# Kernel tuning notes

Hardware: AMD Instinct MI355X
Metric: run time of the kernel (lower is better)

## Reference

```python
import jax, jax.numpy as jnp
import numpy as np

STATE_MASS = 4.0
EPS = 1e-5
LOW_RANK_SCALE = 0.1  # _LOW_RANK_SCALE_INIT


def _ln(x, g, b):
    mu = jnp.mean(x, axis=-1, keepdims=True)
    var = jnp.var(x, axis=-1, keepdims=True)
    return (x - mu) * jax.lax.rsqrt(var + EPS) * g + b


def _signed_abs_softmax(s, axis=-1):
    s = jnp.nan_to_num(s)
    return jnp.sign(s) * jax.nn.softmax(jnp.abs(s), axis=axis)


def _signed_softmax_state(st):
    st = jnp.nan_to_num(st)
    return jnp.sign(st) * jax.nn.softmax(jnp.abs(st), axis=-1) * STATE_MASS


def _low_rank_scores(dst, src, Ut_w, Ut_b, Us_w, Us_b, w):
    # bilinear low-rank pairwise: score[b,i,j] = sum_r (dst_i Ut)_r * w_r * (src_j Us)_r
    pt = dst @ Ut_w + Ut_b                      # [B,Nd,R]
    ps = src @ Us_w + Us_b                      # [B,Ns,R]
    return jnp.einsum('bir,r,bjr->bij', pt, w * LOW_RANK_SCALE, ps)


def _gather_rows(x, idx):
    # x: [B,N,...], idx: [B,M,K] -> [B,M,K,...] (per-batch gather, no NxM broadcast)
    return jax.vmap(lambda xi, ii: xi[ii])(x, idx)


def setup_inputs() -> dict:
    key = jax.random.key(0)
    ks = jax.random.split(key, 8)
    B, S, D, M, R = 16, 2048, 512, 256, 64
    std = 0.02
    return {
        'token_val': jax.random.normal(ks[0], (B, S, D), jnp.float32),
        'token_state': jax.random.normal(ks[1], (B, S), jnp.float32),
        'init_state': jax.random.normal(ks[2], (M,), jnp.float32) * std,
        'init_val': jax.random.normal(ks[3], (M, D), jnp.float32) * std,
        'rUs_w': jax.random.normal(ks[4], (D, R), jnp.float32) * std,
        'rUs_b': jnp.zeros((R,), jnp.float32),
        'rUt_w': jax.random.normal(ks[5], (D, R), jnp.float32) * std,
        'rUt_b': jnp.zeros((R,), jnp.float32),
        'r_w': jnp.ones((R,), jnp.float32),
        'pUs_w': jax.random.normal(ks[6], (D, R), jnp.float32) * std,
        'pUs_b': jnp.zeros((R,), jnp.float32),
        'pUt_w': jax.random.normal(ks[7], (D, R), jnp.float32) * std,
        'pUt_b': jnp.zeros((R,), jnp.float32),
        'p_w': jnp.ones((R,), jnp.float32),
        'ln_g': jnp.ones((D,), jnp.float32),
        'ln_b': jnp.zeros((D,), jnp.float32),
        'topk': 16,
    }


def reference(token_val, token_state, init_state, init_val,
              rUs_w, rUs_b, rUt_w, rUt_b, r_w,
              pUs_w, pUs_b, pUt_w, pUt_b, p_w,
              ln_g, ln_b, topk):
    B = token_val.shape[0]
    M, D = init_val.shape

    # _MemoryLevel.initialize
    mem_state = _signed_softmax_state(jnp.broadcast_to(init_state, (B, M)))
    mem_val = _ln(jnp.broadcast_to(init_val, (B, M, D)), ln_g, ln_b)

    # ---- SparseTransition (write): route tokens -> slots, top-k sources/slot ----
    scores = _low_rank_scores(mem_val, token_val, rUt_w, rUt_b, rUs_w, rUs_b, r_w)  # [B,M,S]
    _, idx = jax.lax.top_k(jnp.abs(scores), topk)              # [B,M,K]
    sel = jnp.take_along_axis(scores, idx, axis=-1)            # [B,M,K]
    edges = _signed_abs_softmax(sel, axis=-1)                  # signed-abs-softmax over edges
    v_sel = _gather_rows(token_val, idx)                       # [B,M,K,D]
    s_sel = _gather_rows(token_state, idx)                     # [B,M,K]
    mem_val = mem_val + jnp.einsum('bmk,bmkd->bmd', edges, v_sel)   # merge_mode='add'
    mem_state = mem_state + jnp.einsum('bmk,bmk->bm', edges, s_sel)
    mem_state = _signed_softmax_state(mem_state)
    mem_val = _ln(mem_val, ln_g, ln_b)

    # ---- SparsePropagation within slots: state-weighted top-k edges, residual ----
    pscores = _low_rank_scores(mem_val, mem_val, pUt_w, pUt_b, pUs_w, pUs_b, p_w)   # [B,M,M]
    pscores = pscores * mem_state[:, None, :]                  # state_weight_edges
    _, pidx = jax.lax.top_k(jnp.abs(pscores), topk)            # [B,M,K]
    psel = jnp.take_along_axis(pscores, pidx, axis=-1)
    pe = _signed_abs_softmax(psel, axis=-1)
    pv = _gather_rows(mem_val, pidx)                           # [B,M,K,D]
    pst = _gather_rows(mem_state, pidx)                        # [B,M,K]
    mem_val = mem_val + jnp.einsum('bmk,bmkd->bmd', pe, pv)    # residual=True
    mem_state = mem_state + jnp.einsum('bmk,bmk->bm', pe, pst)
    mem_state = _signed_softmax_state(mem_state)
    mem_val = _ln(mem_val, ln_g, ln_b)
    return mem_val
```

## Files before the change

kernel.cpp:

```cpp
#include <hip/hip_runtime.h>
#include <hip/hip_bf16.h>
#include <math.h>

#define BB 16
#define SS 2048
#define DD 512
#define MM 256
#define RR 64
#define KK 16
#define GPAD 68

__device__ __forceinline__ float wave_sum(float v) {
#pragma unroll
  for (int off = 32; off > 0; off >>= 1) v += __shfl_xor(v, off);
  return v;
}

__device__ __forceinline__ float sgnf(float v) {
  return (v > 0.f) ? 1.f : ((v < 0.f) ? -1.f : 0.f);
}

__global__ __launch_bounds__(256) void k_init(
    const float* __restrict__ init_val, const float* __restrict__ ln_g,
    const float* __restrict__ ln_b, const float* __restrict__ rUt_w,
    const float* __restrict__ rUt_b, const float* __restrict__ r_w,
    float* __restrict__ mv0, float* __restrict__ pt0) {
  int m = blockIdx.x, t = threadIdx.x;
  __shared__ float row[DD];
  __shared__ float red[8];
  float x0 = init_val[m * DD + t];
  float x1 = init_val[m * DD + t + 256];
  float s = wave_sum(x0 + x1);
  float sq = wave_sum(x0 * x0 + x1 * x1);
  if ((t & 63) == 0) { red[t >> 6] = s; red[4 + (t >> 6)] = sq; }
  __syncthreads();
  float mean = (red[0] + red[1] + red[2] + red[3]) * (1.0f / DD);
  float var = (red[4] + red[5] + red[6] + red[7]) * (1.0f / DD) - mean * mean;
  float rs = rsqrtf(var + 1e-5f);
  float n0 = (x0 - mean) * rs * ln_g[t] + ln_b[t];
  float n1 = (x1 - mean) * rs * ln_g[t + 256] + ln_b[t + 256];
  mv0[m * DD + t] = n0;
  mv0[m * DD + t + 256] = n1;
  row[t] = n0;
  row[t + 256] = n1;
  __syncthreads();
  if (t < RR) {
    float acc = rUt_b[t];
    for (int d = 0; d < DD; ++d) acc += row[d] * rUt_w[d * RR + t];
    pt0[m * RR + t] = acc * r_w[t] * 0.1f;
  }
}

__global__ __launch_bounds__(256) void k_state_softmax(
    const float* __restrict__ in, float* __restrict__ out) {
  int b = blockIdx.x, t = threadIdx.x;
  __shared__ float red[4];
  float v = in[b * MM + t];
  float a = fabsf(v);
  float mx = a;
#pragma unroll
  for (int off = 32; off > 0; off >>= 1) mx = fmaxf(mx, __shfl_xor(mx, off));
  if ((t & 63) == 0) red[t >> 6] = mx;
  __syncthreads();
  mx = fmaxf(fmaxf(red[0], red[1]), fmaxf(red[2], red[3]));
  __syncthreads();
  float e = expf(a - mx);
  float ssum = wave_sum(e);
  if ((t & 63) == 0) red[t >> 6] = ssum;
  __syncthreads();
  ssum = red[0] + red[1] + red[2] + red[3];
  out[b * MM + t] = sgnf(v) * e / ssum * 4.0f;
}

__global__ __launch_bounds__(64) void k_ps(
    const float* __restrict__ A, const float* __restrict__ W,
    const float* __restrict__ bias, float* __restrict__ C0,
    float* __restrict__ C1, float* __restrict__ C2, float* __restrict__ C3) {
  __shared__ float Ast[8][32];
  int t = threadIdx.x;
  int rg = t >> 3;
  int cg = t & 7;
  int q = blockIdx.x >> 10;
  int rt = blockIdx.x & 1023;
  int row0 = rt * 32;
  int k0 = q * 128;
  float* C = (q == 0) ? C0 : (q == 1) ? C1 : (q == 2) ? C2 : C3;
  int lr = t >> 1;
  int ks = (t & 1) * 4;
  float acc[4][8] = {};
  for (int ch = 0; ch < 16; ++ch) {
    int kc = k0 + ch * 8;
    float4 av4 = *reinterpret_cast<const float4*>(
        &A[(size_t)(row0 + lr) * DD + kc + ks]);
    float4 wlo[8], whi[8];
#pragma unroll
    for (int j = 0; j < 8; ++j) {
      const float* wr = W + (size_t)(kc + j) * RR + cg * 8;
      wlo[j] = *reinterpret_cast<const float4*>(wr);
      whi[j] = *reinterpret_cast<const float4*>(wr + 4);
    }
    __syncthreads();
    Ast[ks + 0][lr] = av4.x;
    Ast[ks + 1][lr] = av4.y;
    Ast[ks + 2][lr] = av4.z;
    Ast[ks + 3][lr] = av4.w;
    __syncthreads();
#pragma unroll
    for (int j = 0; j < 8; ++j) {
      float4 a4 = *reinterpret_cast<const float4*>(&Ast[j][rg * 4]);
      float wv[8] = {wlo[j].x, wlo[j].y, wlo[j].z, wlo[j].w,
                     whi[j].x, whi[j].y, whi[j].z, whi[j].w};
      float av[4] = {a4.x, a4.y, a4.z, a4.w};
#pragma unroll
      for (int i = 0; i < 4; ++i)
#pragma unroll
        for (int c = 0; c < 8; ++c) acc[i][c] += av[i] * wv[c];
    }
  }
  float bvx[8];
#pragma unroll
  for (int c = 0; c < 8; ++c) bvx[c] = (q == 0) ? bias[cg * 8 + c] : 0.f;
#pragma unroll
  for (int i = 0; i < 4; ++i) {
    int rr = row0 + rg * 4 + i;
    float4 o0, o1;
    o0.x = acc[i][0] + bvx[0]; o0.y = acc[i][1] + bvx[1];
    o0.z = acc[i][2] + bvx[2]; o0.w = acc[i][3] + bvx[3];
    o1.x = acc[i][4] + bvx[4]; o1.y = acc[i][5] + bvx[5];
    o1.z = acc[i][6] + bvx[6]; o1.w = acc[i][7] + bvx[7];
    *reinterpret_cast<float4*>(&C[(size_t)rr * RR + cg * 8]) = o0;
    *reinterpret_cast<float4*>(&C[(size_t)rr * RR + cg * 8 + 4]) = o1;
  }
}

template <bool TRANS_OUT>
__device__ __forceinline__ void gemm_body(
    const float* __restrict__ A, const float* __restrict__ W,
    const float* __restrict__ bias, const float* __restrict__ colscale,
    float csmul, const float* __restrict__ rowscale, float* __restrict__ C,
    int row0, float (*Ast)[GPAD], float (*Ws)[GPAD]) {
  int tid = threadIdx.x;
  int ty = tid >> 4, tx = tid & 15;
  float acc[4][4] = {};
  for (int kc = 0; kc < DD; kc += 32) {
#pragma unroll
    for (int i = 0; i < 2; ++i) {
      int s4 = i * 256 + tid;
      int r = s4 >> 3;
      int k4 = s4 & 7;
      float4 v = *reinterpret_cast<const float4*>(
          &A[(size_t)(row0 + r) * DD + kc + k4 * 4]);
      Ast[k4 * 4 + 0][r] = v.x;
      Ast[k4 * 4 + 1][r] = v.y;
      Ast[k4 * 4 + 2][r] = v.z;
      Ast[k4 * 4 + 3][r] = v.w;
    }
#pragma unroll
    for (int i = 0; i < 2; ++i) {
      int s4 = i * 256 + tid;
      int r = s4 >> 4;
      int c4 = s4 & 15;
      float4 v = *reinterpret_cast<const float4*>(
          &W[(size_t)(kc + r) * RR + c4 * 4]);
      *reinterpret_cast<float4*>(&Ws[r][c4 * 4]) = v;
    }
    __syncthreads();
#pragma unroll
    for (int k = 0; k < 32; ++k) {
      float4 a4 = *reinterpret_cast<const float4*>(&Ast[k][ty * 4]);
      float4 w4 = *reinterpret_cast<const float4*>(&Ws[k][tx * 4]);
      acc[0][0] += a4.x * w4.x; acc[0][1] += a4.x * w4.y;
      acc[0][2] += a4.x * w4.z; acc[0][3] += a4.x * w4.w;
      acc[1][0] += a4.y * w4.x; acc[1][1] += a4.y * w4.y;
      acc[1][2] += a4.y * w4.z; acc[1][3] += a4.y * w4.w;
      acc[2][0] += a4.z * w4.x; acc[2][1] += a4.z * w4.y;
      acc[2][2] += a4.z * w4.z; acc[2][3] += a4.z * w4.w;
      acc[3][0] += a4.w * w4.x; acc[3][1] += a4.w * w4.y;
      acc[3][2] += a4.w * w4.z; acc[3][3] += a4.w * w4.w;
    }
    __syncthreads();
  }
#pragma unroll
  for (int i = 0; i < 4; ++i) {
    int rr = row0 + ty * 4 + i;
    float rsc = rowscale ? rowscale[rr] : 1.f;
#pragma unroll
    for (int j = 0; j < 4; ++j) {
      int cc = tx * 4 + j;
      float v = acc[i][j] + bias[cc];
      if (colscale) v *= colscale[cc] * csmul;
      v *= rsc;
      if (TRANS_OUT) {
        C[((size_t)(rr >> 8) * RR + cc) * MM + (rr & 255)] = v;
      } else {
        C[(size_t)rr * RR + cc] = v;
      }
    }
  }
}

__global__ __launch_bounds__(256) void k_gemm_pair(
    const float* __restrict__ mv1, const float* __restrict__ pUt_w,
    const float* __restrict__ pUt_b, const float* __restrict__ p_w,
    const float* __restrict__ pUs_w, const float* __restrict__ pUs_b,
    const float* __restrict__ ms1, float* __restrict__ pt1,
    float* __restrict__ ps1T) {
  __shared__ float Ast[32][GPAD];
  __shared__ float Ws[32][GPAD];
  if (blockIdx.x < 64) {
    gemm_body<false>(mv1, pUt_w, pUt_b, p_w, 0.1f, nullptr, pt1,
                     blockIdx.x * 64, Ast, Ws);
  } else {
    gemm_body<true>(mv1, pUs_w, pUs_b, nullptr, 1.f, ms1, ps1T,
                    (blockIdx.x - 64) * 64, Ast, Ws);
  }
}

#define PSW 144
__device__ __forceinline__ int psw(int j) { return j + ((j >> 5) << 2); }

__global__ __launch_bounds__(256) void k_scores(
    const float* __restrict__ pt0, const float* __restrict__ ps0,
    const float* __restrict__ ps1, const float* __restrict__ ps2,
    const float* __restrict__ ps3, float* __restrict__ scores) {
  __shared__ float PtT[RR][128];
  __shared__ float PsT[RR][PSW];
  int t = threadIdx.x;
  int b = blockIdx.z;
  int m0 = blockIdx.y * 128;
  int j0 = blockIdx.x * 128;
#pragma unroll
  for (int ii = 0; ii < 2; ++ii) {
    int slot = ii * 256 + t;
    int tm4 = slot >> 4, tk4 = slot & 15;
    const float* base = pt0 + (size_t)(m0 + tm4 * 4) * RR + tk4 * 4;
    float4 v0 = *reinterpret_cast<const float4*>(base);
    float4 v1 = *reinterpret_cast<const float4*>(base + RR);
    float4 v2 = *reinterpret_cast<const float4*>(base + 2 * RR);
    float4 v3 = *reinterpret_cast<const float4*>(base + 3 * RR);
    float4 w;
    w.x = v0.x; w.y = v1.x; w.z = v2.x; w.w = v3.x;
    *reinterpret_cast<float4*>(&PtT[tk4 * 4 + 0][tm4 * 4]) = w;
    w.x = v0.y; w.y = v1.y; w.z = v2.y; w.w = v3.y;
    *reinterpret_cast<float4*>(&PtT[tk4 * 4 + 1][tm4 * 4]) = w;
    w.x = v0.z; w.y = v1.z; w.z = v2.z; w.w = v3.z;
    *reinterpret_cast<float4*>(&PtT[tk4 * 4 + 2][tm4 * 4]) = w;
    w.x = v0.w; w.y = v1.w; w.z = v2.w; w.w = v3.w;
    *reinterpret_cast<float4*>(&PtT[tk4 * 4 + 3][tm4 * 4]) = w;
  }
#pragma unroll
  for (int ii = 0; ii < 2; ++ii) {
    int slot = ii * 256 + t;
    int jt = slot >> 4, kt = slot & 15;
    size_t off = ((size_t)b * SS + j0 + jt * 4) * RR + kt * 4;
    float4 v0, v1, v2, v3;
    {
      const float* p0 = ps0 + off;
      const float* p1 = ps1 + off;
      const float* p2 = ps2 + off;
      const float* p3 = ps3 + off;
#pragma unroll
      for (int rr2 = 0; rr2 < 4; ++rr2) {
        float4 a = *reinterpret_cast<const float4*>(p0 + rr2 * RR);
        float4 bq = *reinterpret_cast<const float4*>(p1 + rr2 * RR);
        float4 cq = *reinterpret_cast<const float4*>(p2 + rr2 * RR);
        float4 dq = *reinterpret_cast<const float4*>(p3 + rr2 * RR);
        float4 r;
        r.x = a.x + bq.x + cq.x + dq.x;
        r.y = a.y + bq.y + cq.y + dq.y;
        r.z = a.z + bq.z + cq.z + dq.z;
        r.w = a.w + bq.w + cq.w + dq.w;
        if (rr2 == 0) v0 = r; else if (rr2 == 1) v1 = r;
        else if (rr2 == 2) v2 = r; else v3 = r;
      }
    }
    int jc = psw(jt * 4);
    float4 w;
    w.x = v0.x; w.y = v1.x; w.z = v2.x; w.w = v3.x;
    *reinterpret_cast<float4*>(&PsT[kt * 4 + 0][jc]) = w;
    w.x = v0.y; w.y = v1.y; w.z = v2.y; w.w = v3.y;
    *reinterpret_cast<float4*>(&PsT[kt * 4 + 1][jc]) = w;
    w.x = v0.z; w.y = v1.z; w.z = v2.z; w.w = v3.z;
    *reinterpret_cast<float4*>(&PsT[kt * 4 + 2][jc]) = w;
    w.x = v0.w; w.y = v1.w; w.z = v2.w; w.w = v3.w;
    *reinterpret_cast<float4*>(&PsT[kt * 4 + 3][jc]) = w;
  }
  __syncthreads();
  int jg = t & 15;
  int mg = t >> 4;
  int jlo = psw(jg * 8);
  float acc[8][8] = {};
#pragma unroll
  for (int k = 0; k < RR; ++k) {
    float4 a0 = *reinterpret_cast<const float4*>(&PtT[k][mg * 8]);
    float4 a1 = *reinterpret_cast<const float4*>(&PtT[k][mg * 8 + 4]);
    float4 w0 = *reinterpret_cast<const float4*>(&PsT[k][jlo]);
    float4 w1 = *reinterpret_cast<const float4*>(&PsT[k][jlo + 4]);
    float av[8] = {a0.x, a0.y, a0.z, a0.w, a1.x, a1.y, a1.z, a1.w};
    float wv[8] = {w0.x, w0.y, w0.z, w0.w, w1.x, w1.y, w1.z, w1.w};
#pragma unroll
    for (int r = 0; r < 8; ++r)
#pragma unroll
      for (int cc = 0; cc < 8; ++cc) acc[r][cc] += av[r] * wv[cc];
  }
  float* obase =
      scores + (size_t)b * MM * SS + (size_t)(m0 + mg * 8) * SS + j0 + jg * 8;
#pragma unroll
  for (int r = 0; r < 8; ++r) {
    float4 o0, o1;
    o0.x = acc[r][0]; o0.y = acc[r][1]; o0.z = acc[r][2]; o0.w = acc[r][3];
    o1.x = acc[r][4]; o1.y = acc[r][5]; o1.z = acc[r][6]; o1.w = acc[r][7];
    *reinterpret_cast<float4*>(obase + (size_t)r * SS) = o0;
    *reinterpret_cast<float4*>(obase + (size_t)r * SS + 4) = o1;
  }
}

__global__ __launch_bounds__(256) void k_write(
    const float* __restrict__ scores, const float* __restrict__ token_val,
    const float* __restrict__ token_state, const float* __restrict__ mv0,
    const float* __restrict__ ms0, const float* __restrict__ ln_g,
    const float* __restrict__ ln_b, float* __restrict__ mv1,
    float* __restrict__ ms_w) {
  int t = threadIdx.x;
  int wave = t >> 6, lane = t & 63;
  int i = blockIdx.x;
  int slot = i >> 3;
  int b = 2 * (i & 7) + (slot >> 6);
  int m = (slot & 63) * 4 + wave;
  int row = b * MM + m;
  __shared__ float srl[4][SS];
  __shared__ int selj_sh[4][KK];
  float4* srl4 = reinterpret_cast<float4*>(&srl[wave][0]);
  const float* srow = scores + (size_t)row * SS;
  unsigned au[32];
  unsigned maxa = 0u;
#pragma unroll
  for (int ch = 0; ch < 8; ++ch) {
    float4 q = *reinterpret_cast<const float4*>(srow + (ch * 64 + lane) * 4);
    srl4[ch * 64 + lane] = q;
    au[ch * 4 + 0] = __float_as_uint(q.x) & 0x7fffffffu;
    au[ch * 4 + 1] = __float_as_uint(q.y) & 0x7fffffffu;
    au[ch * 4 + 2] = __float_as_uint(q.z) & 0x7fffffffu;
    au[ch * 4 + 3] = __float_as_uint(q.w) & 0x7fffffffu;
    maxa = max(maxa, max(max(au[ch * 4], au[ch * 4 + 1]),
                         max(au[ch * 4 + 2], au[ch * 4 + 3])));
  }
#pragma unroll
  for (int off = 32; off > 0; off >>= 1)
    maxa = max(maxa, (unsigned)__shfl_xor((int)maxa, off));
  unsigned lo = 0u, hi = maxa, thr = 0u;
  bool early = false;
  while (lo < hi) {
    unsigned mid = lo + ((hi - lo + 1u) >> 1);
    int cnt = 0;
#pragma unroll
    for (int c = 0; c < 32; ++c) cnt += __popcll(__ballot(au[c] >= mid));
    if (cnt == KK) { thr = mid; early = true; break; }
    if (cnt > KK) lo = mid; else hi = mid - 1u;
  }
  if (!early) thr = lo;
  unsigned long long ltmask = (1ull << lane) - 1ull;
  int s = 0;
  unsigned tiemask = 0u;
#pragma unroll
  for (int c = 0; c < 32; ++c) {
    bool sg = early ? (au[c] >= thr) : (au[c] > thr);
    unsigned long long mk = __ballot(sg);
    if (sg)
      selj_sh[wave][s + __popcll(mk & ltmask)] =
          (c >> 2) * 256 + lane * 4 + (c & 3);
    s += __popcll(mk);
    if (!early && au[c] == thr) tiemask |= 1u << c;
  }
  int taken = s;
  while (taken < KK) {
    int myj = 0x7fffffff;
#pragma unroll
    for (int c = 0; c < 32; ++c)
      if ((tiemask >> c) & 1u) {
        int j = (c >> 2) * 256 + lane * 4 + (c & 3);
        myj = min(myj, j);
      }
    int wj = myj;
#pragma unroll
    for (int off = 32; off > 0; off >>= 1) wj = min(wj, __shfl_xor(wj, off));
    if (wj == 0x7fffffff) break;
    if (((wj >> 2) & 63) == lane) tiemask &= ~(1u << (((wj >> 8) << 2) | (wj & 3)));
    if (lane == 0) selj_sh[wave][taken] = wj;
    ++taken;
  }
  int js[KK];
  float es[KK];
#pragma unroll
  for (int k = 0; k < KK; ++k) {
    js[k] = selj_sh[wave][k];
    es[k] = srl[wave][js[k]];
  }
  float mx = 0.f;
#pragma unroll
  for (int k = 0; k < KK; ++k) mx = fmaxf(mx, fabsf(es[k]));
  float ssum = 0.f;
#pragma unroll
  for (int k = 0; k < KK; ++k) {
    float ex = expf(fabsf(es[k]) - mx);
    ssum += ex;
    es[k] = sgnf(es[k]) * ex;
  }
  float inv = 1.f / ssum;
  int dbase = lane * 8;
  const float* m0row = mv0 + m * DD + dbase;
  float4 a0 = *reinterpret_cast<const float4*>(m0row);
  float4 a1 = *reinterpret_cast<const float4*>(m0row + 4);
  float acc[8] = {a0.x, a0.y, a0.z, a0.w, a1.x, a1.y, a1.z, a1.w};
  float stacc = 0.f;
#pragma unroll
  for (int k = 0; k < KK; ++k) {
    float e = es[k] * inv;
    const float* tv = token_val + ((size_t)b * SS + js[k]) * DD + dbase;
    float4 u0 = *reinterpret_cast<const float4*>(tv);
    float4 u1 = *reinterpret_cast<const float4*>(tv + 4);
    acc[0] += e * u0.x; acc[1] += e * u0.y; acc[2] += e * u0.z; acc[3] += e * u0.w;
    acc[4] += e * u1.x; acc[5] += e * u1.y; acc[6] += e * u1.z; acc[7] += e * u1.w;
    stacc += e * token_state[(size_t)b * SS + js[k]];
  }
  if (lane == 0) ms_w[row] = ms0[m] + stacc;
  float s1 = 0.f, s2 = 0.f;
#pragma unroll
  for (int c = 0; c < 8; ++c) { s1 += acc[c]; s2 += acc[c] * acc[c]; }
  s1 = wave_sum(s1);
  s2 = wave_sum(s2);
  float mean = s1 * (1.0f / DD);
  float var = s2 * (1.0f / DD) - mean * mean;
  float rs = rsqrtf(var + 1e-5f);
  float4 g0 = *reinterpret_cast<const float4*>(ln_g + dbase);
  float4 g1 = *reinterpret_cast<const float4*>(ln_g + dbase + 4);
  float4 b0v = *reinterpret_cast<const float4*>(ln_b + dbase);
  float4 b1v = *reinterpret_cast<const float4*>(ln_b + dbase + 4);
  float4 o0, o1;
  o0.x = (acc[0] - mean) * rs * g0.x + b0v.x;
  o0.y = (acc[1] - mean) * rs * g0.y + b0v.y;
  o0.z = (acc[2] - mean) * rs * g0.z + b0v.z;
  o0.w = (acc[3] - mean) * rs * g0.w + b0v.w;
  o1.x = (acc[4] - mean) * rs * g1.x + b1v.x;
  o1.y = (acc[5] - mean) * rs * g1.y + b1v.y;
  o1.z = (acc[6] - mean) * rs * g1.z + b1v.z;
  o1.w = (acc[7] - mean) * rs * g1.w + b1v.w;
  float* orow = mv1 + (size_t)row * DD + dbase;
  *reinterpret_cast<float4*>(orow) = o0;
  *reinterpret_cast<float4*>(orow + 4) = o1;
}

__global__ __launch_bounds__(256, 4) void k_prop(
    const float* __restrict__ pt1, const float* __restrict__ ps1T,
    const float* __restrict__ mv1, const float* __restrict__ ln_g,
    const float* __restrict__ ln_b, float* __restrict__ out) {
  int t = threadIdx.x;
  int wave = t >> 6, lane = t & 63;
  int row = blockIdx.x * 4 + wave;
  int b = row >> 8, m = row & 255;
  __shared__ int selj_sh[4][KK];
  __shared__ float selv_sh[4][KK];
  float ptval = pt1[(size_t)row * RR + lane];
  const float* pB = ps1T + (size_t)b * RR * MM + lane * 4;
  float sc[4] = {0.f, 0.f, 0.f, 0.f};
#pragma unroll 8
  for (int r = 0; r < RR; ++r) {
    float w = __shfl(ptval, r);
    float4 pv = *reinterpret_cast<const float4*>(pB + r * MM);
    sc[0] += w * pv.x; sc[1] += w * pv.y; sc[2] += w * pv.z; sc[3] += w * pv.w;
  }
  int jbase = lane * 4;
  unsigned au[4];
#pragma unroll
  for (int c = 0; c < 4; ++c) au[c] = __float_as_uint(sc[c]) & 0x7fffffffu;
  unsigned lo = 0u, hi = 0x7f800000u, thr = 0u;
  bool early = false;
  while (lo < hi) {
    unsigned mid = lo + ((hi - lo + 1u) >> 1);
    int cnt = 0;
#pragma unroll
    for (int c = 0; c < 4; ++c) cnt += __popcll(__ballot(au[c] >= mid));
    if (cnt == KK) { thr = mid; early = true; break; }
    if (cnt > KK) lo = mid; else hi = mid - 1u;
  }
  if (!early) thr = lo;
  unsigned long long ltmask = (1ull << lane) - 1ull;
  int s = 0;
  unsigned tiemask = 0u;
#pragma unroll
  for (int c = 0; c < 4; ++c) {
    bool sg = early ? (au[c] >= thr) : (au[c] > thr);
    unsigned long long mk = __ballot(sg);
    if (sg) {
      int slot = s + __popcll(mk & ltmask);
      selj_sh[wave][slot] = jbase + c;
      selv_sh[wave][slot] = sc[c];
    }
    s += __popcll(mk);
    if (!early && au[c] == thr) tiemask |= 1u << c;
  }
  int taken = s;
  while (taken < KK) {
    int myj = 0x7fffffff;
#pragma unroll
    for (int c = 0; c < 4; ++c)
      if ((tiemask >> c) & 1u) myj = min(myj, jbase + c);
    int wj = myj;
#pragma unroll
    for (int off = 32; off > 0; off >>= 1) wj = min(wj, __shfl_xor(wj, off));
    if (wj == 0x7fffffff) break;
    if (wj >= jbase && wj < jbase + 4) {
      tiemask &= ~(1u << (wj - jbase));
      selv_sh[wave][taken] = sc[wj - jbase];
      if (lane == (wj >> 2)) selj_sh[wave][taken] = wj;
    }
    ++taken;
  }
  int js[KK];
  float es[KK];
#pragma unroll
  for (int k = 0; k < KK; ++k) { js[k] = selj_sh[wave][k]; es[k] = selv_sh[wave][k]; }
  float mx = 0.f;
#pragma unroll
  for (int k = 0; k < KK; ++k) mx = fmaxf(mx, fabsf(es[k]));
  float ssum = 0.f;
#pragma unroll
  for (int k = 0; k < KK; ++k) {
    float ex = expf(fabsf(es[k]) - mx);
    ssum += ex;
    es[k] = sgnf(es[k]) * ex;
  }
  float inv = 1.f / ssum;
  int dbase = lane * 8;
  const float* mrow = mv1 + (size_t)row * DD + dbase;
  float4 a0 = *reinterpret_cast<const float4*>(mrow);
  float4 a1 = *reinterpret_cast<const float4*>(mrow + 4);
  float acc[8] = {a0.x, a0.y, a0.z, a0.w, a1.x, a1.y, a1.z, a1.w};
#pragma unroll
  for (int k = 0; k < KK; ++k) {
    float e = es[k] * inv;
    const float* pv = mv1 + ((size_t)b * MM + js[k]) * DD + dbase;
    float4 u0 = *reinterpret_cast<const float4*>(pv);
    float4 u1 = *reinterpret_cast<const float4*>(pv + 4);
    acc[0] += e * u0.x; acc[1] += e * u0.y; acc[2] += e * u0.z; acc[3] += e * u0.w;
    acc[4] += e * u1.x; acc[5] += e * u1.y; acc[6] += e * u1.z; acc[7] += e * u1.w;
  }
  float s1 = 0.f, s2 = 0.f;
#pragma unroll
  for (int c = 0; c < 8; ++c) { s1 += acc[c]; s2 += acc[c] * acc[c]; }
  s1 = wave_sum(s1);
  s2 = wave_sum(s2);
  float mean = s1 * (1.0f / DD);
  float var = s2 * (1.0f / DD) - mean * mean;
  float rs = rsqrtf(var + 1e-5f);
  float4 g0 = *reinterpret_cast<const float4*>(ln_g + dbase);
  float4 g1 = *reinterpret_cast<const float4*>(ln_g + dbase + 4);
  float4 b0v = *reinterpret_cast<const float4*>(ln_b + dbase);
  float4 b1v = *reinterpret_cast<const float4*>(ln_b + dbase + 4);
  float4 o0, o1;
  o0.x = (acc[0] - mean) * rs * g0.x + b0v.x;
  o0.y = (acc[1] - mean) * rs * g0.y + b0v.y;
  o0.z = (acc[2] - mean) * rs * g0.z + b0v.z;
  o0.w = (acc[3] - mean) * rs * g0.w + b0v.w;
  o1.x = (acc[4] - mean) * rs * g1.x + b1v.x;
  o1.y = (acc[5] - mean) * rs * g1.y + b1v.y;
  o1.z = (acc[6] - mean) * rs * g1.z + b1v.z;
  o1.w = (acc[7] - mean) * rs * g1.w + b1v.w;
  float* orow = out + (size_t)row * DD + dbase;
  *reinterpret_cast<float4*>(orow) = o0;
  *reinterpret_cast<float4*>(orow + 4) = o1;
}

extern "C" void kernel_launch(void* const* d_in, const int* in_sizes, int n_in,
                              void* d_out, int out_size, void* d_ws,
                              size_t ws_size, hipStream_t stream) {
  const float* token_val = (const float*)d_in[0];
  const float* token_state = (const float*)d_in[1];
  const float* init_state = (const float*)d_in[2];
  const float* init_val = (const float*)d_in[3];
  const float* rUs_w = (const float*)d_in[4];
  const float* rUs_b = (const float*)d_in[5];
  const float* rUt_w = (const float*)d_in[6];
  const float* rUt_b = (const float*)d_in[7];
  const float* r_w = (const float*)d_in[8];
  const float* pUs_w = (const float*)d_in[9];
  const float* pUs_b = (const float*)d_in[10];
  const float* pUt_w = (const float*)d_in[11];
  const float* pUt_b = (const float*)d_in[12];
  const float* p_w = (const float*)d_in[13];
  const float* ln_g = (const float*)d_in[14];
  const float* ln_b = (const float*)d_in[15];
  float* out = (float*)d_out;

  float* ws = (float*)d_ws;
  float* mv0 = ws;    ws += MM * DD;
  float* pt0 = ws;    ws += MM * RR;
  float* ms0 = ws;    ws += MM;
  float* ps = ws;     ws += (size_t)BB * SS * RR;
  float* scores = ws; ws += (size_t)BB * MM * SS;
  float* mv1 = ws;    ws += (size_t)BB * MM * DD;
  float* ms_w = ws;   ws += BB * MM;
  float* ms1 = ws;    ws += BB * MM;
  float* pt1 = ws;    ws += (size_t)BB * MM * RR;
  float* ps1T = ws;   ws += (size_t)BB * RR * MM;
  float* ps2 = ws;    ws += (size_t)BB * SS * RR;
  float* psB = mv1;
  float* psD = out;

  k_init<<<MM, 256, 0, stream>>>(init_val, ln_g, ln_b, rUt_w, rUt_b, r_w, mv0, pt0);
  k_state_softmax<<<1, 256, 0, stream>>>(init_state, ms0);
  k_ps<<<4096, 64, 0, stream>>>(token_val, rUs_w, rUs_b, ps, psB, ps2, psD);
  dim3 gs(SS / 128, MM / 128, BB);
  k_scores<<<gs, 256, 0, stream>>>(pt0, ps, psB, ps2, psD, scores);
  k_write<<<(BB * MM) / 4, 256, 0, stream>>>(scores, token_val, token_state,
                                             mv0, ms0, ln_g, ln_b, mv1, ms_w);
  k_state_softmax<<<BB, 256, 0, stream>>>(ms_w, ms1);
  k_gemm_pair<<<128, 256, 0, stream>>>(mv1, pUt_w, pUt_b, p_w, pUs_w, pUs_b,
                                       ms1, pt1, ps1T);
  k_prop<<<(BB * MM) / 4, 256, 0, stream>>>(pt1, ps1T, mv1, ln_g, ln_b, out);
}
```

Baseline: 173.1 us.

## Replace split-K token projection with full-K GEMM, fuse init softmax, drop score LDS staging

The token projection GEMM no longer splits K into four partial outputs that k_scores had to sum; it now reuses the shared 64x64 tiled gemm_body over the full K dimension with float4 stores. The initial state softmax is folded into block 0 of k_init, which removes one launch. k_write stops staging each full score row in LDS and rereads the 16 selected scores from global memory instead. These changes cut partial-sum traffic, one launch and LDS pressure, but the new projection launches only 512 blocks.

```diff
diff --git a/kernel.cpp b/kernel.cpp
--- a/kernel.cpp
+++ b/kernel.cpp
@@ -21,13 +21,33 @@
 }
 
 __global__ __launch_bounds__(256) void k_init(
-    const float* __restrict__ init_val, const float* __restrict__ ln_g,
-    const float* __restrict__ ln_b, const float* __restrict__ rUt_w,
-    const float* __restrict__ rUt_b, const float* __restrict__ r_w,
-    float* __restrict__ mv0, float* __restrict__ pt0) {
+    const float* __restrict__ init_val, const float* __restrict__ init_state,
+    const float* __restrict__ ln_g, const float* __restrict__ ln_b,
+    const float* __restrict__ rUt_w, const float* __restrict__ rUt_b,
+    const float* __restrict__ r_w, float* __restrict__ mv0,
+    float* __restrict__ pt0, float* __restrict__ ms0) {
   int m = blockIdx.x, t = threadIdx.x;
   __shared__ float row[DD];
   __shared__ float red[8];
+  __shared__ float red2[4];
+  if (blockIdx.x == 0) {
+    float v = init_state[t];
+    float a = fabsf(v);
+    float mx = a;
+#pragma unroll
+    for (int off = 32; off > 0; off >>= 1) mx = fmaxf(mx, __shfl_xor(mx, off));
+    if ((t & 63) == 0) red2[t >> 6] = mx;
+    __syncthreads();
+    mx = fmaxf(fmaxf(red2[0], red2[1]), fmaxf(red2[2], red2[3]));
+    __syncthreads();
+    float e = expf(a - mx);
+    float ssum = wave_sum(e);
+    if ((t & 63) == 0) red2[t >> 6] = ssum;
+    __syncthreads();
+    ssum = red2[0] + red2[1] + red2[2] + red2[3];
+    ms0[t] = sgnf(v) * e / ssum * 4.0f;
+    __syncthreads();
+  }
   float x0 = init_val[m * DD + t];
   float x1 = init_val[m * DD + t + 256];
   float s = wave_sum(x0 + x1);
@@ -72,67 +92,6 @@
   out[b * MM + t] = sgnf(v) * e / ssum * 4.0f;
 }
 
-__global__ __launch_bounds__(64) void k_ps(
-    const float* __restrict__ A, const float* __restrict__ W,
-    const float* __restrict__ bias, float* __restrict__ C0,
-    float* __restrict__ C1, float* __restrict__ C2, float* __restrict__ C3) {
-  __shared__ float Ast[8][32];
-  int t = threadIdx.x;
-  int rg = t >> 3;
-  int cg = t & 7;
-  int q = blockIdx.x >> 10;
-  int rt = blockIdx.x & 1023;
-  int row0 = rt * 32;
-  int k0 = q * 128;
-  float* C = (q == 0) ? C0 : (q == 1) ? C1 : (q == 2) ? C2 : C3;
-  int lr = t >> 1;
-  int ks = (t & 1) * 4;
-  float acc[4][8] = {};
-  for (int ch = 0; ch < 16; ++ch) {
-    int kc = k0 + ch * 8;
-    float4 av4 = *reinterpret_cast<const float4*>(
-        &A[(size_t)(row0 + lr) * DD + kc + ks]);
-    float4 wlo[8], whi[8];
-#pragma unroll
-    for (int j = 0; j < 8; ++j) {
-      const float* wr = W + (size_t)(kc + j) * RR + cg * 8;
-      wlo[j] = *reinterpret_cast<const float4*>(wr);
-      whi[j] = *reinterpret_cast<const float4*>(wr + 4);
-    }
-    __syncthreads();
-    Ast[ks + 0][lr] = av4.x;
-    Ast[ks + 1][lr] = av4.y;
-    Ast[ks + 2][lr] = av4.z;
-    Ast[ks + 3][lr] = av4.w;
-    __syncthreads();
-#pragma unroll
-    for (int j = 0; j < 8; ++j) {
-      float4 a4 = *reinterpret_cast<const float4*>(&Ast[j][rg * 4]);
-      float wv[8] = {wlo[j].x, wlo[j].y, wlo[j].z, wlo[j].w,
-                     whi[j].x, whi[j].y, whi[j].z, whi[j].w};
-      float av[4] = {a4.x, a4.y, a4.z, a4.w};
-#pragma unroll
-      for (int i = 0; i < 4; ++i)
-#pragma unroll
-        for (int c = 0; c < 8; ++c) acc[i][c] += av[i] * wv[c];
-    }
-  }
-  float bvx[8];
-#pragma unroll
-  for (int c = 0; c < 8; ++c) bvx[c] = (q == 0) ? bias[cg * 8 + c] : 0.f;
-#pragma unroll
-  for (int i = 0; i < 4; ++i) {
-    int rr = row0 + rg * 4 + i;
-    float4 o0, o1;
-    o0.x = acc[i][0] + bvx[0]; o0.y = acc[i][1] + bvx[1];
-    o0.z = acc[i][2] + bvx[2]; o0.w = acc[i][3] + bvx[3];
-    o1.x = acc[i][4] + bvx[4]; o1.y = acc[i][5] + bvx[5];
-    o1.z = acc[i][6] + bvx[6]; o1.w = acc[i][7] + bvx[7];
-    *reinterpret_cast<float4*>(&C[(size_t)rr * RR + cg * 8]) = o0;
-    *reinterpret_cast<float4*>(&C[(size_t)rr * RR + cg * 8 + 4]) = o1;
-  }
-}
-
 template <bool TRANS_OUT>
 __device__ __forceinline__ void gemm_body(
     const float* __restrict__ A, const float* __restrict__ W,
@@ -184,19 +143,38 @@
   for (int i = 0; i < 4; ++i) {
     int rr = row0 + ty * 4 + i;
     float rsc = rowscale ? rowscale[rr] : 1.f;
-#pragma unroll
-    for (int j = 0; j < 4; ++j) {
-      int cc = tx * 4 + j;
-      float v = acc[i][j] + bias[cc];
-      if (colscale) v *= colscale[cc] * csmul;
-      v *= rsc;
-      if (TRANS_OUT) {
+    if (TRANS_OUT) {
+#pragma unroll
+      for (int j = 0; j < 4; ++j) {
+        int cc = tx * 4 + j;
+        float v = acc[i][j] + bias[cc];
+        if (colscale) v *= colscale[cc] * csmul;
+        v *= rsc;
         C[((size_t)(rr >> 8) * RR + cc) * MM + (rr & 255)] = v;
-      } else {
-        C[(size_t)rr * RR + cc] = v;
       }
+    } else {
+      float4 o;
+      o.x = acc[i][0] + bias[tx * 4];
+      o.y = acc[i][1] + bias[tx * 4 + 1];
+      o.z = acc[i][2] + bias[tx * 4 + 2];
+      o.w = acc[i][3] + bias[tx * 4 + 3];
+      if (colscale) {
+        o.x *= colscale[tx * 4] * csmul; o.y *= colscale[tx * 4 + 1] * csmul;
+        o.z *= colscale[tx * 4 + 2] * csmul; o.w *= colscale[tx * 4 + 3] * csmul;
+      }
+      o.x *= rsc; o.y *= rsc; o.z *= rsc; o.w *= rsc;
+      *reinterpret_cast<float4*>(&C[(size_t)rr * RR + tx * 4]) = o;
     }
   }
+}
+
+__global__ __launch_bounds__(256) void k_ps(
+    const float* __restrict__ A, const float* __restrict__ W,
+    const float* __restrict__ bias, float* __restrict__ C) {
+  __shared__ float Ast[32][GPAD];
+  __shared__ float Ws[32][GPAD];
+  gemm_body<false>(A, W, bias, nullptr, 1.f, nullptr, C, blockIdx.x * 64,
+                   Ast, Ws);
 }
 
 __global__ __launch_bounds__(256) void k_gemm_pair(
@@ -220,9 +198,8 @@
 __device__ __forceinline__ int psw(int j) { return j + ((j >> 5) << 2); }
 
 __global__ __launch_bounds__(256) void k_scores(
-    const float* __restrict__ pt0, const float* __restrict__ ps0,
-    const float* __restrict__ ps1, const float* __restrict__ ps2,
-    const float* __restrict__ ps3, float* __restrict__ scores) {
+    const float* __restrict__ pt0, const float* __restrict__ ps,
+    float* __restrict__ scores) {
   __shared__ float PtT[RR][128];
   __shared__ float PsT[RR][PSW];
   int t = threadIdx.x;
@@ -252,28 +229,11 @@
   for (int ii = 0; ii < 2; ++ii) {
     int slot = ii * 256 + t;
     int jt = slot >> 4, kt = slot & 15;
-    size_t off = ((size_t)b * SS + j0 + jt * 4) * RR + kt * 4;
-    float4 v0, v1, v2, v3;
-    {
-      const float* p0 = ps0 + off;
-      const float* p1 = ps1 + off;
-      const float* p2 = ps2 + off;
-      const float* p3 = ps3 + off;
-#pragma unroll
-      for (int rr2 = 0; rr2 < 4; ++rr2) {
-        float4 a = *reinterpret_cast<const float4*>(p0 + rr2 * RR);
-        float4 bq = *reinterpret_cast<const float4*>(p1 + rr2 * RR);
-        float4 cq = *reinterpret_cast<const float4*>(p2 + rr2 * RR);
-        float4 dq = *reinterpret_cast<const float4*>(p3 + rr2 * RR);
-        float4 r;
-        r.x = a.x + bq.x + cq.x + dq.x;
-        r.y = a.y + bq.y + cq.y + dq.y;
-        r.z = a.z + bq.z + cq.z + dq.z;
-        r.w = a.w + bq.w + cq.w + dq.w;
-        if (rr2 == 0) v0 = r; else if (rr2 == 1) v1 = r;
-        else if (rr2 == 2) v2 = r; else v3 = r;
-      }
-    }
+    const float* base = ps + ((size_t)b * SS + j0 + jt * 4) * RR + kt * 4;
+    float4 v0 = *reinterpret_cast<const float4*>(base);
+    float4 v1 = *reinterpret_cast<const float4*>(base + RR);
+    float4 v2 = *reinterpret_cast<const float4*>(base + 2 * RR);
+    float4 v3 = *reinterpret_cast<const float4*>(base + 3 * RR);
     int jc = psw(jt * 4);
     float4 w;
     w.x = v0.x; w.y = v1.x; w.z = v2.x; w.w = v3.x;
@@ -328,16 +288,13 @@
   int b = 2 * (i & 7) + (slot >> 6);
   int m = (slot & 63) * 4 + wave;
   int row = b * MM + m;
-  __shared__ float srl[4][SS];
   __shared__ int selj_sh[4][KK];
-  float4* srl4 = reinterpret_cast<float4*>(&srl[wave][0]);
   const float* srow = scores + (size_t)row * SS;
   unsigned au[32];
   unsigned maxa = 0u;
 #pragma unroll
   for (int ch = 0; ch < 8; ++ch) {
     float4 q = *reinterpret_cast<const float4*>(srow + (ch * 64 + lane) * 4);
-    srl4[ch * 64 + lane] = q;
     au[ch * 4 + 0] = __float_as_uint(q.x) & 0x7fffffffu;
     au[ch * 4 + 1] = __float_as_uint(q.y) & 0x7fffffffu;
     au[ch * 4 + 2] = __float_as_uint(q.z) & 0x7fffffffu;
@@ -394,7 +351,7 @@
 #pragma unroll
   for (int k = 0; k < KK; ++k) {
     js[k] = selj_sh[wave][k];
-    es[k] = srl[wave][js[k]];
+    es[k] = srow[js[k]];
   }
   float mx = 0.f;
 #pragma unroll
@@ -603,15 +560,12 @@
   float* ms1 = ws;    ws += BB * MM;
   float* pt1 = ws;    ws += (size_t)BB * MM * RR;
   float* ps1T = ws;   ws += (size_t)BB * RR * MM;
-  float* ps2 = ws;    ws += (size_t)BB * SS * RR;
-  float* psB = mv1;
-  float* psD = out;
-
-  k_init<<<MM, 256, 0, stream>>>(init_val, ln_g, ln_b, rUt_w, rUt_b, r_w, mv0, pt0);
-  k_state_softmax<<<1, 256, 0, stream>>>(init_state, ms0);
-  k_ps<<<4096, 64, 0, stream>>>(token_val, rUs_w, rUs_b, ps, psB, ps2, psD);
+
+  k_init<<<MM, 256, 0, stream>>>(init_val, init_state, ln_g, ln_b, rUt_w,
+                                 rUt_b, r_w, mv0, pt0, ms0);
+  k_ps<<<(BB * SS) / 64, 256, 0, stream>>>(token_val, rUs_w, rUs_b, ps);
   dim3 gs(SS / 128, MM / 128, BB);
-  k_scores<<<gs, 256, 0, stream>>>(pt0, ps, psB, ps2, psD, scores);
+  k_scores<<<gs, 256, 0, stream>>>(pt0, ps, scores);
   k_write<<<(BB * MM) / 4, 256, 0, stream>>>(scores, token_val, token_state,
                                              mv0, ms0, ln_g, ln_b, mv1, ms_w);
   k_state_softmax<<<BB, 256, 0, stream>>>(ms_w, ms1);
```

Measured after the change: 159.2 us. -8.0%, faster.
